# Kernel optimization log

Hardware: AMD Instinct MI355X
Metric: run time of the kernel (lower is better)

The kernel has to match this reference:

```python
import jax, jax.numpy as jnp
import numpy as np

B = 64          # batch of graphs
N_GOALS = 16
N_SHELVES = 112
N = N_GOALS + N_SHELVES   # 128 nodes per graph
L = 5           # num_layers
D = 32          # node_embedding_dim
DE = 32         # edge_embedding_dim
DT = 32         # timestep_embedding_dim
D_MSG_IN = 2 * D + DT + 1  # 97


def setup_inputs() -> dict:
    key = jax.random.key(0)
    ks = iter(jax.random.split(key, 40))
    def nrm(shape, s=0.05):
        return jax.random.normal(next(ks), shape, jnp.float32) * s
    inp = {}
    inp["pos"] = jax.random.uniform(next(ks), (B, N_SHELVES, 2), jnp.float32, -1.0, 1.0)
    inp["timesteps"] = jax.random.randint(next(ks), (B,), 0, 1000)
    inp["goal_pos"] = jax.random.uniform(next(ks), (N_GOALS, 2), jnp.float32, -1.0, 1.0)
    inp["W_hin"] = nrm((2, D));            inp["b_hin"] = nrm((D,))
    inp["W_msg1"] = nrm((L, D_MSG_IN, DE)); inp["b_msg1"] = nrm((L, DE))
    inp["W_msg2"] = nrm((L, DE, DE));       inp["b_msg2"] = nrm((L, DE))
    inp["W_att"] = nrm((L, DE, 1));         inp["b_att"] = nrm((L, 1))
    inp["W_pos1"] = nrm((L, DE, DE));       inp["b_pos1"] = nrm((L, DE))
    inp["W_pos2"] = nrm((L, DE, 1));        inp["b_pos2"] = nrm((L, 1))
    inp["W_node1"] = nrm((L - 1, DE + D, D)); inp["b_node1"] = nrm((L - 1, D))
    inp["W_node2"] = nrm((L - 1, D, D));      inp["b_node2"] = nrm((L - 1, D))
    inp["W_t"] = nrm((L - 1, DT, DT));        inp["b_t"] = nrm((L - 1, DT))
    return inp


def _forward(pos, timesteps, goal_pos, W_hin, b_hin, W_msg1, b_msg1, W_msg2, b_msg2,
             W_att, b_att, W_pos1, b_pos1, W_pos2, b_pos2,
             W_node1, b_node1, W_node2, b_node2, W_t, b_t):
    silu = jax.nn.silu
    b = pos.shape[0]
    n_g = goal_pos.shape[0]
    n_sh = pos.shape[1]
    n = n_g + n_sh
    num_layers = W_msg1.shape[0]

    # fully-connected edge template per graph (PyG: edge_index[0]=src=row, edge_index[1]=dst=col)
    src_l = jnp.repeat(jnp.arange(n), n)
    dst_l = jnp.tile(jnp.arange(n), n)
    offs = (jnp.arange(b) * n)[:, None]
    src = (offs + src_l[None, :]).reshape(-1)   # [b*n*n]
    dst = (offs + dst_l[None, :]).reshape(-1)
    e_batch = jnp.repeat(jnp.arange(b), n * n)  # batch[edge_index[0]]

    # node one-hot features: goals [1,0], shelves [0,1]
    h0 = jnp.concatenate([
        jnp.tile(jnp.array([1.0, 0.0], jnp.float32), (n_g, 1)),
        jnp.tile(jnp.array([0.0, 1.0], jnp.float32), (n_sh, 1)),
    ], axis=0)                                   # [n, 2]
    x = jnp.tile(h0, (b, 1))                     # [b*n, 2]

    # node positions: goal positions (shared template) then shelf positions
    p = jnp.concatenate([jnp.broadcast_to(goal_pos, (b, n_g, 2)), pos], axis=1).reshape(-1, 2)

    # sinusoidal timestep embedding
    dt = b_t.shape[-1]
    half = dt // 2
    freqs = jnp.exp(-jnp.log(10000.0) * jnp.arange(half, dtype=jnp.float32) / half)
    ang = timesteps.astype(jnp.float32)[:, None] * freqs[None, :]
    temb = jnp.concatenate([jnp.cos(ang), jnp.sin(ang)], axis=-1)  # [b, dt]

    h = x @ W_hin + b_hin  # [b*n, D]

    for i in range(num_layers):
        te = temb[e_batch]                       # [E, dt]
        pd = p[dst] - p[src]                     # pos_i - pos_j
        radial = jnp.sum(pd * pd, axis=-1, keepdims=True)
        pd = pd / (jax.lax.stop_gradient(jnp.sqrt(radial)) + 1e-6)
        m = jnp.concatenate([h[dst], h[src], radial, te], axis=-1)  # [E, 97]
        m = silu(m @ W_msg1[i] + b_msg1[i])
        m = silu(m @ W_msg2[i] + b_msg2[i])
        m = m * jax.nn.sigmoid(m @ W_att[i] + b_att[i])             # attention gate
        pw = silu(m @ W_pos1[i] + b_pos1[i]) @ W_pos2[i] + b_pos2[i]  # [E, 1]
        aggr_h = jax.ops.segment_sum(m, dst, num_segments=b * n)    # scatter-add
        # scatter-mean: every node receives exactly n incoming edges (fully connected incl. self-loop)
        aggr_p = jax.ops.segment_sum(pd * pw, dst, num_segments=b * n) / n
        if i < num_layers - 1:
            u = silu(jnp.concatenate([h, aggr_h], axis=-1) @ W_node1[i] + b_node1[i])
            u = u @ W_node2[i] + b_node2[i]
            h = jnp.where(u > 0, u, 0.01 * u) + h   # LeakyReLU + residual
            temb = silu(temb @ W_t[i] + b_t[i])
        p = aggr_p + p

    return p.reshape(b, n, 2)[:, n_g:, :].reshape(pos.shape)


def reference(pos, timesteps, goal_pos, W_hin, b_hin, W_msg1, b_msg1, W_msg2, b_msg2,
              W_att, b_att, W_pos1, b_pos1, W_pos2, b_pos2,
              W_node1, b_node1, W_node2, b_node2, W_t, b_t):
    return _forward(pos, timesteps, goal_pos, W_hin, b_hin, W_msg1, b_msg1, W_msg2, b_msg2,
                    W_att, b_att, W_pos1, b_pos1, W_pos2, b_pos2,
                    W_node1, b_node1, W_node2, b_node2, W_t, b_t)
```

## Files before the change

### kernel.cpp

```cpp
#include <hip/hip_runtime.h>
#include <hip/hip_bf16.h>

constexpr int B = 64;
constexpr int NG = 16;
constexpr int NSH = 112;
constexpr int N = 128;
constexpr int NN = B * N;
constexpr int L = 5;

constexpr int OFF_H     = 0;
constexpr int OFF_P     = OFF_H + NN * 32;
constexpr int OFF_TEMB0 = OFF_P + NN * 2;
constexpr int OFF_TEMB1 = OFF_TEMB0 + B * 32;
constexpr int OFF_HA    = OFF_TEMB1 + B * 32;
constexpr int OFF_HB    = OFF_HA + NN * 32;
constexpr int OFF_AGH   = OFF_HB + NN * 32;
constexpr int OFF_AGP   = OFF_AGH + NN * 32;

typedef __attribute__((ext_vector_type(8))) short bf16x8;
typedef __attribute__((ext_vector_type(4))) float f32x4;

__device__ __forceinline__ float fsigmoid(float x) {
    return __builtin_amdgcn_rcpf(1.0f + __expf(-x));
}
__device__ __forceinline__ float fsilu(float x) { return x * fsigmoid(x); }
__device__ __forceinline__ short f2bfs(float f) {
    union { __hip_bfloat16 b; short s; } u; u.b = __float2bfloat16(f); return u.s;
}
__device__ __forceinline__ float bf2f(unsigned short u) {
    union { unsigned int i; float f; } v; v.i = ((unsigned int)u) << 16; return v.f;
}
__device__ __forceinline__ unsigned int pk_trunc(float lo, float hi) {
    union { float f; unsigned int u; } a, b;
    a.f = hi; b.f = lo;
    return __builtin_amdgcn_perm(a.u, b.u, 0x07060302u);
}

__global__ __launch_bounds__(256) void setup_kernel(
    const float* __restrict__ pos, const int* __restrict__ timesteps,
    const float* __restrict__ goal_pos,
    const float* __restrict__ W_hin, const float* __restrict__ b_hin,
    float* __restrict__ ws)
{
    int idx = blockIdx.x * 256 + threadIdx.x;

    if (idx < NN * 32) {
        int c = idx & 31; int node = idx >> 5; int local = node & 127;
        int row = (local < NG) ? 0 : 1;
        ws[OFF_H + idx] = W_hin[row * 32 + c] + b_hin[c];
        return;
    }
    idx -= NN * 32;
    if (idx < NN * 2) {
        int d = idx & 1; int node = idx >> 1; int g = node >> 7; int local = node & 127;
        float v = (local < NG) ? goal_pos[local * 2 + d]
                               : pos[(g * NSH + (local - NG)) * 2 + d];
        ws[OFF_P + idx] = v;
        return;
    }
    idx -= NN * 2;
    if (idx < B * 32) {
        int j = idx & 31; int g = idx >> 5;
        float t = (float)timesteps[g];
        int jj = (j < 16) ? j : (j - 16);
        float freq = expf(-logf(10000.0f) * (float)jj / 16.0f);
        float ang = t * freq;
        ws[OFF_TEMB0 + idx] = (j < 16) ? cosf(ang) : sinf(ang);
    }
}

__global__ __launch_bounds__(256) void pre_kernel(
    float* __restrict__ R,
    const float* __restrict__ W_msg1, const float* __restrict__ b_msg1,
    const float* __restrict__ tembIn, int layer)
{
    int tid = blockIdx.x * 256 + threadIdx.x;
    int c = tid & 31; int node = tid >> 5; int g = node >> 7;
    const float* __restrict__ W1 = W_msg1 + layer * 97 * 32;
    float accA = b_msg1[layer * 32 + c];
    float accB = 0.f;
#pragma unroll
    for (int k = 0; k < 32; ++k) {
        float hk = R[OFF_H + node * 32 + k];
        accA += hk * W1[k * 32 + c];
        accB += hk * W1[(32 + k) * 32 + c];
    }
#pragma unroll
    for (int k = 0; k < 32; ++k)
        accA += tembIn[g * 32 + k] * W1[(65 + k) * 32 + c];
    R[OFF_HA + tid] = accA;
    ((unsigned short*)(R + OFF_HB))[tid] = (unsigned short)f2bfs(accB);
}

__global__ __attribute__((amdgpu_flat_work_group_size(256, 256)))
__attribute__((amdgpu_waves_per_eu(2, 4))) void edge_kernel(
    float* __restrict__ R,
    const float* __restrict__ W_msg1,
    const float* __restrict__ W_msg2, const float* __restrict__ b_msg2,
    const float* __restrict__ W_att, const float* __restrict__ b_att,
    const float* __restrict__ W_pos1, const float* __restrict__ b_pos1,
    const float* __restrict__ W_pos2, const float* __restrict__ b_pos2,
    float* __restrict__ aggh, float* __restrict__ aggp,
    float* __restrict__ out, int layer)
{
    __shared__ unsigned short sHBh[128 * 40];
    __shared__ float sPx[128], sPy[128];
    __shared__ unsigned int mbuf[4 * 16 * 20];
    __shared__ float2 spn[4][64];

    const int t = threadIdx.x;
    const int bx = blockIdx.x;
    const int g = bx >> 5;
    const int gbase = g * 128;

    const unsigned short* HBH = (const unsigned short*)(R + OFF_HB);
#pragma unroll
    for (int ch = 0; ch < 2; ++ch) {
        int chunk = t + ch * 256;
        int row = chunk >> 2, g4 = chunk & 3;
        uint4 v = *(const uint4*)(HBH + (gbase + row) * 32 + (g4 << 3));
        *(uint4*)(sHBh + row * 40 + (g4 << 3)) = v;
    }
    if (t < 128) {
        sPx[t] = R[OFF_P + (gbase + t) * 2];
        sPy[t] = R[OFF_P + (gbase + t) * 2 + 1];
    }
    __syncthreads();

    const int lane = t & 63, w = t >> 6;
    const int c = lane & 15;
    const int rg = lane >> 4;
    const int kk = rg << 3;
    const int dloc = ((bx & 31) << 2) | w;
    const int dstNode = gbase + dloc;

    const float* __restrict__ Wm2L = W_msg2 + layer * 1024;
    const float* __restrict__ Wp1L = W_pos1 + layer * 1024;
    bf16x8 WB1c0, WB1c1, WBpc0, WBpc1, WBac;
#pragma unroll
    for (int j = 0; j < 8; ++j) {
        WB1c0[j] = f2bfs(Wm2L[(kk + j) * 32 + c]);
        WB1c1[j] = f2bfs(Wm2L[(kk + j) * 32 + c + 16]);
        int pk = ((kk + j) & 1) * 16 + ((kk + j) >> 1);
        WBpc0[j] = f2bfs(Wp1L[pk * 32 + c]);
        WBpc1[j] = f2bfs(Wp1L[pk * 32 + c + 16]);
        WBac[j]  = f2bfs(W_att[layer * 32 + pk]);
    }

    float vha[8], vwr[8];
    {
        const float* haR = R + OFF_HA + dstNode * 32 + kk;
        const float* wrR = W_msg1 + layer * 97 * 32 + 64 * 32 + kk;
#pragma unroll
        for (int j = 0; j < 8; ++j) { vha[j] = haR[j]; vwr[j] = wrR[j]; }
    }
    const float batt   = b_att[layer];
    const float vbm20  = b_msg2[layer * 32 + c], vbm21 = b_msg2[layer * 32 + c + 16];
    const float vbp10  = b_pos1[layer * 32 + c], vbp11 = b_pos1[layer * 32 + c + 16];
    const float vwp20  = W_pos2[layer * 32 + c], vwp21 = W_pos2[layer * 32 + c + 16];
    const float bp2    = b_pos2[layer];
    const float pxd = R[OFF_P + dstNode * 2], pyd = R[OFF_P + dstNode * 2 + 1];

    unsigned int* mb = mbuf + w * 16 * 20;

    float aghc0 = 0.f, aghc1 = 0.f, apx = 0.f, apy = 0.f, spnx = 0.f, spny = 0.f;

#pragma unroll 1
    for (int half = 0; half < 2; ++half) {
        const int src = (half << 6) + lane;
        const float dx = pxd - sPx[src];
        const float dy = pyd - sPy[src];
        const float radial = dx * dx + dy * dy;
        const float inv = __builtin_amdgcn_rcpf(__builtin_amdgcn_sqrtf(radial) + 1e-6f);
        const float pnx = dx * inv, pny = dy * inv;
        spnx += pnx; spny += pny;
        spn[w][lane] = (float2){pnx, pny};

#pragma unroll
        for (int tt = 0; tt < 4; ++tt) {
            const float rad_t = __shfl(radial, c + (tt << 4));
            uint4 hraw = *(const uint4*)(sHBh + ((half << 6) + c + (tt << 4)) * 40 + kk);
            const unsigned short* hs = (const unsigned short*)&hraw;
            float x[8];
#pragma unroll
            for (int j = 0; j < 8; ++j)
                x[j] = fsilu(vha[j] + bf2f(hs[j]) + rad_t * vwr[j]);
            union { unsigned int u[4]; bf16x8 v; } af;
#pragma unroll
            for (int d = 0; d < 4; ++d) af.u[d] = pk_trunc(x[2 * d], x[2 * d + 1]);
            f32x4 a0 = (f32x4){vbm20, vbm20, vbm20, vbm20};
            f32x4 a1 = (f32x4){vbm21, vbm21, vbm21, vbm21};
            a0 = __builtin_amdgcn_mfma_f32_16x16x32_bf16(af.v, WB1c0, a0, 0, 0, 0);
            a1 = __builtin_amdgcn_mfma_f32_16x16x32_bf16(af.v, WB1c1, a1, 0, 0, 0);

            float s0[4], s1[4];
#pragma unroll
            for (int j = 0; j < 4; ++j) {
                s0[j] = fsilu(a0[j]);
                s1[j] = fsilu(a1[j]);
                mb[((rg << 2) + j) * 20 + c] = pk_trunc(s0[j], s1[j]);
            }

            union { uint4 u; bf16x8 v; } qa;
            qa.u = *(const uint4*)(mb + c * 20 + (rg << 2));
            f32x4 za = (f32x4){batt, batt, batt, batt};
            f32x4 z0 = (f32x4){0.f, 0.f, 0.f, 0.f};
            f32x4 z1 = (f32x4){0.f, 0.f, 0.f, 0.f};
            za = __builtin_amdgcn_mfma_f32_16x16x32_bf16(qa.v, WBac,  za, 0, 0, 0);
            z0 = __builtin_amdgcn_mfma_f32_16x16x32_bf16(qa.v, WBpc0, z0, 0, 0, 0);
            z1 = __builtin_amdgcn_mfma_f32_16x16x32_bf16(qa.v, WBpc1, z1, 0, 0, 0);
#pragma unroll
            for (int j = 0; j < 4; ++j) {
                const float att = fsigmoid(za[j]);
                aghc0 += att * s0[j];
                aghc1 += att * s1[j];
                const float q0 = fsilu(att * z0[j] + vbp10);
                const float q1 = fsilu(att * z1[j] + vbp11);
                const float pwp = q0 * vwp20 + q1 * vwp21;
                const float2 pn = spn[w][(tt << 4) + (rg << 2) + j];
                apx += pwp * pn.x;
                apy += pwp * pn.y;
            }
        }
    }

    aghc0 += __shfl_xor(aghc0, 16); aghc0 += __shfl_xor(aghc0, 32);
    aghc1 += __shfl_xor(aghc1, 16); aghc1 += __shfl_xor(aghc1, 32);
#pragma unroll
    for (int off = 1; off < 64; off <<= 1) {
        apx  += __shfl_xor(apx, off);
        apy  += __shfl_xor(apy, off);
        spnx += __shfl_xor(spnx, off);
        spny += __shfl_xor(spny, off);
    }
    if (layer < L - 1) {
        if (lane < 16)       aggh[dstNode * 32 + lane] = aghc0;
        else if (lane < 32)  aggh[dstNode * 32 + lane] = aghc1;
        if (lane == 0) {
            aggp[dstNode * 2]     = (apx + bp2 * spnx) * (1.0f / 128.0f);
            aggp[dstNode * 2 + 1] = (apy + bp2 * spny) * (1.0f / 128.0f);
        }
    } else if (lane == 0 && dloc >= NG) {
        out[(g * NSH + (dloc - NG)) * 2]     = pxd + (apx + bp2 * spnx) * (1.0f / 128.0f);
        out[(g * NSH + (dloc - NG)) * 2 + 1] = pyd + (apy + bp2 * spny) * (1.0f / 128.0f);
    }
}

__global__ __attribute__((amdgpu_flat_work_group_size(64, 64)))
__attribute__((amdgpu_waves_per_eu(2, 4))) void node_kernel(
    float* __restrict__ ws,
    const float* __restrict__ W_node1, const float* __restrict__ b_node1,
    const float* __restrict__ W_node2, const float* __restrict__ b_node2,
    const float* __restrict__ W_t, const float* __restrict__ b_t,
    const float* __restrict__ W_msg1, const float* __restrict__ b_msg1,
    int layer)
{
    __shared__ float sH[16][36];
    __shared__ float sAG[16][36];
    __shared__ unsigned int mb[16 * 20];

    const int lane = threadIdx.x;
    const int bx = blockIdx.x;
    const int nbase = bx << 4;
    const int g = bx >> 3;
    const int c = lane & 15, rg = lane >> 4, kk = rg << 3;

    {
        const int row = lane >> 2, seg = lane & 3;
        const float* hsrc = ws + OFF_H + (nbase + row) * 32 + (seg << 3);
        const float* asrc = ws + OFF_AGH + (nbase + row) * 32 + (seg << 3);
#pragma unroll
        for (int j = 0; j < 8; ++j) {
            sH[row][(seg << 3) + j]  = hsrc[j];
            sAG[row][(seg << 3) + j] = asrc[j];
        }
    }

    const float* __restrict__ Wn1 = W_node1 + layer * 2048;
    const float* __restrict__ Wn2 = W_node2 + layer * 1024;
    const float* __restrict__ W1  = W_msg1 + (layer + 1) * 97 * 32;
    bf16x8 B1[2][2], B2[2], Ba[2], Bb[2];
#pragma unroll
    for (int j = 0; j < 8; ++j) {
        const int pk = ((kk + j) & 1) * 16 + ((kk + j) >> 1);
#pragma unroll
        for (int nh = 0; nh < 2; ++nh) {
            B1[0][nh][j] = f2bfs(Wn1[(kk + j) * 32 + nh * 16 + c]);
            B1[1][nh][j] = f2bfs(Wn1[(32 + kk + j) * 32 + nh * 16 + c]);
            B2[nh][j]    = f2bfs(Wn2[pk * 32 + nh * 16 + c]);
            Ba[nh][j]    = f2bfs(W1[pk * 32 + nh * 16 + c]);
            Bb[nh][j]    = f2bfs(W1[(32 + pk) * 32 + nh * 16 + c]);
        }
    }

    const int c2 = lane & 31;
    const float* __restrict__ tin = ws + ((layer & 1) ? OFF_TEMB1 : OFF_TEMB0) + g * 32;
    const float* __restrict__ Wt = W_t + layer * 1024;
    float a2 = b_t[layer * 32 + c2];
#pragma unroll
    for (int k = 0; k < 32; ++k) a2 += tin[k] * Wt[k * 32 + c2];
    const float tnew = fsilu(a2);
    float tv = b_msg1[(layer + 1) * 32 + c2];
#pragma unroll
    for (int k = 0; k < 32; ++k) tv += __shfl(tnew, k) * W1[(65 + k) * 32 + c2];
    if ((bx & 7) == 0 && lane < 32)
        ws[((layer & 1) ? OFF_TEMB0 : OFF_TEMB1) + g * 32 + lane] = tnew;

    union { unsigned int u[4]; bf16x8 v; } A0, A1;
#pragma unroll
    for (int d = 0; d < 4; ++d) {
        A0.u[d] = pk_trunc(sH[c][kk + 2 * d],  sH[c][kk + 2 * d + 1]);
        A1.u[d] = pk_trunc(sAG[c][kk + 2 * d], sAG[c][kk + 2 * d + 1]);
    }
    f32x4 u1[2];
#pragma unroll
    for (int nh = 0; nh < 2; ++nh) {
        const float bb = b_node1[layer * 32 + nh * 16 + c];
        f32x4 acc = (f32x4){bb, bb, bb, bb};
        acc = __builtin_amdgcn_mfma_f32_16x16x32_bf16(A0.v, B1[0][nh], acc, 0, 0, 0);
        acc = __builtin_amdgcn_mfma_f32_16x16x32_bf16(A1.v, B1[1][nh], acc, 0, 0, 0);
        u1[nh] = acc;
    }

#pragma unroll
    for (int j = 0; j < 4; ++j)
        mb[((rg << 2) + j) * 20 + c] = pk_trunc(fsilu(u1[0][j]), fsilu(u1[1][j]));
    union { uint4 q; bf16x8 v; } qa;
    qa.q = *(const uint4*)(mb + c * 20 + (rg << 2));
    f32x4 u2[2];
#pragma unroll
    for (int nh = 0; nh < 2; ++nh) {
        const float bb = b_node2[layer * 32 + nh * 16 + c];
        f32x4 acc = (f32x4){bb, bb, bb, bb};
        u2[nh] = __builtin_amdgcn_mfma_f32_16x16x32_bf16(qa.v, B2[nh], acc, 0, 0, 0);
    }

    float hp0[4], hp1[4];
#pragma unroll
    for (int j = 0; j < 4; ++j) {
        const int row = (rg << 2) + j;
        const float h0 = sH[row][c], h1 = sH[row][c + 16];
        const float v0 = u2[0][j], v1 = u2[1][j];
        hp0[j] = (v0 > 0.f ? v0 : 0.01f * v0) + h0;
        hp1[j] = (v1 > 0.f ? v1 : 0.01f * v1) + h1;
        ws[OFF_H + (nbase + row) * 32 + c]      = hp0[j];
        ws[OFF_H + (nbase + row) * 32 + c + 16] = hp1[j];
        mb[row * 20 + c] = pk_trunc(hp0[j], hp1[j]);
    }

    qa.q = *(const uint4*)(mb + c * 20 + (rg << 2));
    f32x4 ha[2], hb[2];
    {
        f32x4 zz = (f32x4){0.f, 0.f, 0.f, 0.f};
#pragma unroll
        for (int nh = 0; nh < 2; ++nh) {
            ha[nh] = __builtin_amdgcn_mfma_f32_16x16x32_bf16(qa.v, Ba[nh], zz, 0, 0, 0);
            hb[nh] = __builtin_amdgcn_mfma_f32_16x16x32_bf16(qa.v, Bb[nh], zz, 0, 0, 0);
        }
    }
    const float tv0 = __shfl(tv, c), tv1 = __shfl(tv, c + 16);
    unsigned short* HBH = (unsigned short*)(ws + OFF_HB);
#pragma unroll
    for (int j = 0; j < 4; ++j) {
        const int node = nbase + (rg << 2) + j;
        ws[OFF_HA + node * 32 + c]      = ha[0][j] + tv0;
        ws[OFF_HA + node * 32 + c + 16] = ha[1][j] + tv1;
        HBH[node * 32 + c]      = (unsigned short)f2bfs(hb[0][j]);
        HBH[node * 32 + c + 16] = (unsigned short)f2bfs(hb[1][j]);
    }

    if (lane < 32) {
        const int node = nbase + (lane >> 1), d = lane & 1;
        ws[OFF_P + node * 2 + d] += ws[OFF_AGP + node * 2 + d];
    }
}

extern "C" void kernel_launch(void* const* d_in, const int* in_sizes, int n_in,
                              void* d_out, int out_size, void* d_ws, size_t ws_size,
                              hipStream_t stream)
{
    const float* pos      = (const float*)d_in[0];
    const int*   tsteps   = (const int*)d_in[1];
    const float* goal_pos = (const float*)d_in[2];
    const float* W_hin    = (const float*)d_in[3];
    const float* b_hin    = (const float*)d_in[4];
    const float* W_msg1   = (const float*)d_in[5];
    const float* b_msg1   = (const float*)d_in[6];
    const float* W_msg2   = (const float*)d_in[7];
    const float* b_msg2   = (const float*)d_in[8];
    const float* W_att    = (const float*)d_in[9];
    const float* b_att    = (const float*)d_in[10];
    const float* W_pos1   = (const float*)d_in[11];
    const float* b_pos1   = (const float*)d_in[12];
    const float* W_pos2   = (const float*)d_in[13];
    const float* b_pos2   = (const float*)d_in[14];
    const float* W_node1  = (const float*)d_in[15];
    const float* b_node1  = (const float*)d_in[16];
    const float* W_node2  = (const float*)d_in[17];
    const float* b_node2  = (const float*)d_in[18];
    const float* W_t      = (const float*)d_in[19];
    const float* b_t      = (const float*)d_in[20];

    float* ws = (float*)d_ws;

    constexpr int setup_threads = NN * 32 + NN * 2 + B * 32;
    setup_kernel<<<(setup_threads + 255) / 256, 256, 0, stream>>>(
        pos, tsteps, goal_pos, W_hin, b_hin, ws);
    pre_kernel<<<NN * 32 / 256, 256, 0, stream>>>(ws, W_msg1, b_msg1, ws + OFF_TEMB0, 0);

    for (int l = 0; l < L; ++l) {
        edge_kernel<<<2048, 256, 0, stream>>>(ws, W_msg1, W_msg2, b_msg2, W_att, b_att,
                                              W_pos1, b_pos1, W_pos2, b_pos2,
                                              ws + OFF_AGH, ws + OFF_AGP,
                                              (float*)d_out, l);
        if (l < L - 1)
            node_kernel<<<512, 64, 0, stream>>>(ws, W_node1, b_node1, W_node2,
                                                b_node2, W_t, b_t, W_msg1, b_msg1, l);
    }
}
```

Baseline: 293.4 us.

## Fuse node update into edge kernel and merge setup with pre-projection

Fuses the per-layer node update into the tail of the edge kernel. Each block now handles 16 destination nodes, looping over four per wave, and keeps the aggregates in shared memory instead of writing them to global buffers. HA, HB and position buffers are double-buffered by layer parity so one block's writes do not race with other blocks' reads. The setup and first-layer pre-projection kernels are merged, which removes kernel launches and global round trips. In exchange the grid shrinks from 2048 to 512 blocks, with a serial loop over destinations and a 64-thread node-update tail, so parallelism drops.

Result: faster. 287.2 us, median of 2 (-2.1%).

```diff
diff --git a/kernel.cpp b/kernel.cpp
--- a/kernel.cpp
+++ b/kernel.cpp
@@ -9,13 +9,14 @@
 constexpr int L = 5;
 
 constexpr int OFF_H     = 0;
-constexpr int OFF_P     = OFF_H + NN * 32;
-constexpr int OFF_TEMB0 = OFF_P + NN * 2;
+constexpr int OFF_P0    = OFF_H + NN * 32;
+constexpr int OFF_P1    = OFF_P0 + NN * 2;
+constexpr int OFF_TEMB0 = OFF_P1 + NN * 2;
 constexpr int OFF_TEMB1 = OFF_TEMB0 + B * 32;
-constexpr int OFF_HA    = OFF_TEMB1 + B * 32;
-constexpr int OFF_HB    = OFF_HA + NN * 32;
-constexpr int OFF_AGH   = OFF_HB + NN * 32;
-constexpr int OFF_AGP   = OFF_AGH + NN * 32;
+constexpr int OFF_HA0   = OFF_TEMB1 + B * 32;
+constexpr int OFF_HA1   = OFF_HA0 + NN * 32;
+constexpr int OFF_HB0   = OFF_HA1 + NN * 32;
+constexpr int OFF_HB1   = OFF_HB0 + NN * 16;
 
 typedef __attribute__((ext_vector_type(8))) short bf16x8;
 typedef __attribute__((ext_vector_type(4))) float f32x4;
@@ -36,342 +37,337 @@
     return __builtin_amdgcn_perm(a.u, b.u, 0x07060302u);
 }
 
-__global__ __launch_bounds__(256) void setup_kernel(
-    const float* __restrict__ pos, const int* __restrict__ timesteps,
+__global__ __launch_bounds__(256) void setup_pre_kernel(
+    float* __restrict__ ws,
+    const float* __restrict__ pos, const int* __restrict__ tsteps,
     const float* __restrict__ goal_pos,
     const float* __restrict__ W_hin, const float* __restrict__ b_hin,
-    float* __restrict__ ws)
+    const float* __restrict__ W_msg1, const float* __restrict__ b_msg1)
 {
-    int idx = blockIdx.x * 256 + threadIdx.x;
-
-    if (idx < NN * 32) {
-        int c = idx & 31; int node = idx >> 5; int local = node & 127;
-        int row = (local < NG) ? 0 : 1;
-        ws[OFF_H + idx] = W_hin[row * 32 + c] + b_hin[c];
-        return;
-    }
-    idx -= NN * 32;
-    if (idx < NN * 2) {
-        int d = idx & 1; int node = idx >> 1; int g = node >> 7; int local = node & 127;
-        float v = (local < NG) ? goal_pos[local * 2 + d]
-                               : pos[(g * NSH + (local - NG)) * 2 + d];
-        ws[OFF_P + idx] = v;
-        return;
-    }
-    idx -= NN * 2;
-    if (idx < B * 32) {
-        int j = idx & 31; int g = idx >> 5;
-        float t = (float)timesteps[g];
-        int jj = (j < 16) ? j : (j - 16);
-        float freq = expf(-logf(10000.0f) * (float)jj / 16.0f);
-        float ang = t * freq;
-        ws[OFF_TEMB0 + idx] = (j < 16) ? cosf(ang) : sinf(ang);
-    }
-}
-
-__global__ __launch_bounds__(256) void pre_kernel(
-    float* __restrict__ R,
-    const float* __restrict__ W_msg1, const float* __restrict__ b_msg1,
-    const float* __restrict__ tembIn, int layer)
-{
-    int tid = blockIdx.x * 256 + threadIdx.x;
-    int c = tid & 31; int node = tid >> 5; int g = node >> 7;
-    const float* __restrict__ W1 = W_msg1 + layer * 97 * 32;
-    float accA = b_msg1[layer * 32 + c];
-    float accB = 0.f;
+    __shared__ float sT[32];
+    const int t = threadIdx.x, bx = blockIdx.x;
+    const int tid = bx * 256 + t;
+    const int c = tid & 31, node = tid >> 5, g = node >> 7, local = node & 127;
+    const int row = (local < NG) ? 0 : 1;
+
+    if (t < 32) {
+        const float tf = (float)tsteps[g];
+        const int jj = (t < 16) ? t : (t - 16);
+        const float ang = tf * expf(-logf(10000.0f) * (float)jj / 16.0f);
+        sT[t] = (t < 16) ? cosf(ang) : sinf(ang);
+    }
+    __syncthreads();
+    if ((bx & 15) == 0 && t < 32) ws[OFF_TEMB0 + g * 32 + t] = sT[t];
+
+    ws[OFF_H + tid] = W_hin[row * 32 + c] + b_hin[c];
+
+    if (tid < NN * 2) {
+        const int d = tid & 1, nd = tid >> 1, g0 = nd >> 7, loc = nd & 127;
+        ws[OFF_P0 + tid] = (loc < NG) ? goal_pos[loc * 2 + d]
+                                      : pos[(g0 * NSH + (loc - NG)) * 2 + d];
+    }
+
+    const float* __restrict__ W1 = W_msg1;
+    float accA = b_msg1[c], accB = 0.f;
 #pragma unroll
     for (int k = 0; k < 32; ++k) {
-        float hk = R[OFF_H + node * 32 + k];
+        const float hk = W_hin[row * 32 + k] + b_hin[k];
         accA += hk * W1[k * 32 + c];
         accB += hk * W1[(32 + k) * 32 + c];
     }
 #pragma unroll
     for (int k = 0; k < 32; ++k)
-        accA += tembIn[g * 32 + k] * W1[(65 + k) * 32 + c];
-    R[OFF_HA + tid] = accA;
-    ((unsigned short*)(R + OFF_HB))[tid] = (unsigned short)f2bfs(accB);
+        accA += sT[k] * W1[(65 + k) * 32 + c];
+    ws[OFF_HA0 + tid] = accA;
+    ((unsigned short*)(ws + OFF_HB0))[tid] = (unsigned short)f2bfs(accB);
 }
 
 __global__ __attribute__((amdgpu_flat_work_group_size(256, 256)))
 __attribute__((amdgpu_waves_per_eu(2, 4))) void edge_kernel(
-    float* __restrict__ R,
-    const float* __restrict__ W_msg1,
+    float* __restrict__ ws,
+    const float* __restrict__ W_msg1, const float* __restrict__ b_msg1,
     const float* __restrict__ W_msg2, const float* __restrict__ b_msg2,
     const float* __restrict__ W_att, const float* __restrict__ b_att,
     const float* __restrict__ W_pos1, const float* __restrict__ b_pos1,
     const float* __restrict__ W_pos2, const float* __restrict__ b_pos2,
-    float* __restrict__ aggh, float* __restrict__ aggp,
-    float* __restrict__ out, int layer)
+    const float* __restrict__ W_node1, const float* __restrict__ b_node1,
+    const float* __restrict__ W_node2, const float* __restrict__ b_node2,
+    const float* __restrict__ W_t, const float* __restrict__ b_t,
+    float* __restrict__ out, int l)
 {
     __shared__ unsigned short sHBh[128 * 40];
     __shared__ float sPx[128], sPy[128];
-    __shared__ unsigned int mbuf[4 * 16 * 20];
-    __shared__ float2 spn[4][64];
+    __shared__ __align__(16) unsigned char uraw[7168];
+    __shared__ float sAgg[16][36];
+    __shared__ float2 sAgp[16];
+
+    unsigned int* mbuf = (unsigned int*)uraw;
+    float2* spn = (float2*)(uraw + 5120);
+    float (*sH)[36] = (float(*)[36])uraw;
+    unsigned int* nmb = (unsigned int*)(uraw + 2304);
 
     const int t = threadIdx.x;
     const int bx = blockIdx.x;
-    const int g = bx >> 5;
-    const int gbase = g * 128;
-
-    const unsigned short* HBH = (const unsigned short*)(R + OFF_HB);
+    const int g = bx >> 3, qp = bx & 7;
+    const int gbase = g << 7;
+    const int par = l & 1, op = (l + 1) & 1;
+
+    const float* __restrict__ HAin = ws + (par ? OFF_HA1 : OFF_HA0);
+    const unsigned short* __restrict__ HBin = (const unsigned short*)(ws + (par ? OFF_HB1 : OFF_HB0));
+    const float* __restrict__ Pin = ws + (par ? OFF_P1 : OFF_P0);
+
 #pragma unroll
     for (int ch = 0; ch < 2; ++ch) {
-        int chunk = t + ch * 256;
-        int row = chunk >> 2, g4 = chunk & 3;
-        uint4 v = *(const uint4*)(HBH + (gbase + row) * 32 + (g4 << 3));
-        *(uint4*)(sHBh + row * 40 + (g4 << 3)) = v;
+        const int chunk = t + (ch << 8);
+        const int row = chunk >> 2, g4 = chunk & 3;
+        *(uint4*)(sHBh + row * 40 + (g4 << 3)) =
+            *(const uint4*)(HBin + (gbase + row) * 32 + (g4 << 3));
     }
     if (t < 128) {
-        sPx[t] = R[OFF_P + (gbase + t) * 2];
-        sPy[t] = R[OFF_P + (gbase + t) * 2 + 1];
+        sPx[t] = Pin[(gbase + t) * 2];
+        sPy[t] = Pin[(gbase + t) * 2 + 1];
     }
     __syncthreads();
 
     const int lane = t & 63, w = t >> 6;
-    const int c = lane & 15;
-    const int rg = lane >> 4;
-    const int kk = rg << 3;
-    const int dloc = ((bx & 31) << 2) | w;
-    const int dstNode = gbase + dloc;
-
-    const float* __restrict__ Wm2L = W_msg2 + layer * 1024;
-    const float* __restrict__ Wp1L = W_pos1 + layer * 1024;
+    const int c = lane & 15, rg = lane >> 4, kk = rg << 3;
+
+    const float* __restrict__ Wm2L = W_msg2 + l * 1024;
+    const float* __restrict__ Wp1L = W_pos1 + l * 1024;
     bf16x8 WB1c0, WB1c1, WBpc0, WBpc1, WBac;
 #pragma unroll
     for (int j = 0; j < 8; ++j) {
         WB1c0[j] = f2bfs(Wm2L[(kk + j) * 32 + c]);
         WB1c1[j] = f2bfs(Wm2L[(kk + j) * 32 + c + 16]);
-        int pk = ((kk + j) & 1) * 16 + ((kk + j) >> 1);
+        const int pk = ((kk + j) & 1) * 16 + ((kk + j) >> 1);
         WBpc0[j] = f2bfs(Wp1L[pk * 32 + c]);
         WBpc1[j] = f2bfs(Wp1L[pk * 32 + c + 16]);
-        WBac[j]  = f2bfs(W_att[layer * 32 + pk]);
-    }
-
-    float vha[8], vwr[8];
+        WBac[j]  = f2bfs(W_att[l * 32 + pk]);
+    }
+    float vwr[8];
     {
-        const float* haR = R + OFF_HA + dstNode * 32 + kk;
-        const float* wrR = W_msg1 + layer * 97 * 32 + 64 * 32 + kk;
-#pragma unroll
-        for (int j = 0; j < 8; ++j) { vha[j] = haR[j]; vwr[j] = wrR[j]; }
-    }
-    const float batt   = b_att[layer];
-    const float vbm20  = b_msg2[layer * 32 + c], vbm21 = b_msg2[layer * 32 + c + 16];
-    const float vbp10  = b_pos1[layer * 32 + c], vbp11 = b_pos1[layer * 32 + c + 16];
-    const float vwp20  = W_pos2[layer * 32 + c], vwp21 = W_pos2[layer * 32 + c + 16];
-    const float bp2    = b_pos2[layer];
-    const float pxd = R[OFF_P + dstNode * 2], pyd = R[OFF_P + dstNode * 2 + 1];
+        const float* wrR = W_msg1 + l * 97 * 32 + 64 * 32 + kk;
+#pragma unroll
+        for (int j = 0; j < 8; ++j) vwr[j] = wrR[j];
+    }
+    const float batt  = b_att[l];
+    const float vbm20 = b_msg2[l * 32 + c], vbm21 = b_msg2[l * 32 + c + 16];
+    const float vbp10 = b_pos1[l * 32 + c], vbp11 = b_pos1[l * 32 + c + 16];
+    const float vwp20 = W_pos2[l * 32 + c], vwp21 = W_pos2[l * 32 + c + 16];
+    const float bp2   = b_pos2[l];
 
     unsigned int* mb = mbuf + w * 16 * 20;
 
-    float aghc0 = 0.f, aghc1 = 0.f, apx = 0.f, apy = 0.f, spnx = 0.f, spny = 0.f;
-
 #pragma unroll 1
-    for (int half = 0; half < 2; ++half) {
-        const int src = (half << 6) + lane;
-        const float dx = pxd - sPx[src];
-        const float dy = pyd - sPy[src];
-        const float radial = dx * dx + dy * dy;
-        const float inv = __builtin_amdgcn_rcpf(__builtin_amdgcn_sqrtf(radial) + 1e-6f);
-        const float pnx = dx * inv, pny = dy * inv;
-        spnx += pnx; spny += pny;
-        spn[w][lane] = (float2){pnx, pny};
-
-#pragma unroll
-        for (int tt = 0; tt < 4; ++tt) {
-            const float rad_t = __shfl(radial, c + (tt << 4));
-            uint4 hraw = *(const uint4*)(sHBh + ((half << 6) + c + (tt << 4)) * 40 + kk);
-            const unsigned short* hs = (const unsigned short*)&hraw;
-            float x[8];
-#pragma unroll
-            for (int j = 0; j < 8; ++j)
-                x[j] = fsilu(vha[j] + bf2f(hs[j]) + rad_t * vwr[j]);
-            union { unsigned int u[4]; bf16x8 v; } af;
-#pragma unroll
-            for (int d = 0; d < 4; ++d) af.u[d] = pk_trunc(x[2 * d], x[2 * d + 1]);
-            f32x4 a0 = (f32x4){vbm20, vbm20, vbm20, vbm20};
-            f32x4 a1 = (f32x4){vbm21, vbm21, vbm21, vbm21};
-            a0 = __builtin_amdgcn_mfma_f32_16x16x32_bf16(af.v, WB1c0, a0, 0, 0, 0);
-            a1 = __builtin_amdgcn_mfma_f32_16x16x32_bf16(af.v, WB1c1, a1, 0, 0, 0);
-
-            float s0[4], s1[4];
-#pragma unroll
-            for (int j = 0; j < 4; ++j) {
-                s0[j] = fsilu(a0[j]);
-                s1[j] = fsilu(a1[j]);
-                mb[((rg << 2) + j) * 20 + c] = pk_trunc(s0[j], s1[j]);
+    for (int si = 0; si < 4; ++si) {
+        const int dl = (si << 2) + w;
+        const int dloc = (qp << 4) + dl;
+        const int dstNode = gbase + dloc;
+        float vha[8];
+        {
+            const float* haR = HAin + dstNode * 32 + kk;
+#pragma unroll
+            for (int j = 0; j < 8; ++j) vha[j] = haR[j];
+        }
+        const float pxd = sPx[dloc], pyd = sPy[dloc];
+
+        float aghc0 = 0.f, aghc1 = 0.f, apx = 0.f, apy = 0.f;
+        float spnx = 0.f, spny = 0.f;
+
+#pragma unroll 1
+        for (int half = 0; half < 2; ++half) {
+            const int src = (half << 6) + lane;
+            const float dx = pxd - sPx[src];
+            const float dy = pyd - sPy[src];
+            const float radial = dx * dx + dy * dy;
+            const float inv = __builtin_amdgcn_rcpf(__builtin_amdgcn_sqrtf(radial) + 1e-6f);
+            const float pnx = dx * inv, pny = dy * inv;
+            spnx += pnx; spny += pny;
+            spn[w * 64 + lane] = (float2){pnx, pny};
+
+#pragma unroll
+            for (int tt = 0; tt < 4; ++tt) {
+                const float rad_t = __shfl(radial, c + (tt << 4));
+                uint4 hraw = *(const uint4*)(sHBh + ((half << 6) + c + (tt << 4)) * 40 + kk);
+                const unsigned short* hs = (const unsigned short*)&hraw;
+                float x[8];
+#pragma unroll
+                for (int j = 0; j < 8; ++j)
+                    x[j] = fsilu(vha[j] + bf2f(hs[j]) + rad_t * vwr[j]);
+                union { unsigned int u[4]; bf16x8 v; } af;
+#pragma unroll
+                for (int d = 0; d < 4; ++d) af.u[d] = pk_trunc(x[2 * d], x[2 * d + 1]);
+                f32x4 a0 = (f32x4){vbm20, vbm20, vbm20, vbm20};
+                f32x4 a1 = (f32x4){vbm21, vbm21, vbm21, vbm21};
+                a0 = __builtin_amdgcn_mfma_f32_16x16x32_bf16(af.v, WB1c0, a0, 0, 0, 0);
+                a1 = __builtin_amdgcn_mfma_f32_16x16x32_bf16(af.v, WB1c1, a1, 0, 0, 0);
+
+                float s0[4], s1[4];
+#pragma unroll
+                for (int j = 0; j < 4; ++j) {
+                    s0[j] = fsilu(a0[j]);
+                    s1[j] = fsilu(a1[j]);
+                    mb[((rg << 2) + j) * 20 + c] = pk_trunc(s0[j], s1[j]);
+                }
+
+                union { uint4 u; bf16x8 v; } qa;
+                qa.u = *(const uint4*)(mb + c * 20 + (rg << 2));
+                f32x4 za = (f32x4){batt, batt, batt, batt};
+                f32x4 z0 = (f32x4){0.f, 0.f, 0.f, 0.f};
+                f32x4 z1 = (f32x4){0.f, 0.f, 0.f, 0.f};
+                za = __builtin_amdgcn_mfma_f32_16x16x32_bf16(qa.v, WBac,  za, 0, 0, 0);
+                z0 = __builtin_amdgcn_mfma_f32_16x16x32_bf16(qa.v, WBpc0, z0, 0, 0, 0);
+                z1 = __builtin_amdgcn_mfma_f32_16x16x32_bf16(qa.v, WBpc1, z1, 0, 0, 0);
+#pragma unroll
+                for (int j = 0; j < 4; ++j) {
+                    const float att = fsigmoid(za[j]);
+                    aghc0 += att * s0[j];
+                    aghc1 += att * s1[j];
+                    const float q0 = fsilu(att * z0[j] + vbp10);
+                    const float q1 = fsilu(att * z1[j] + vbp11);
+                    const float pwp = q0 * vwp20 + q1 * vwp21;
+                    const float2 pn = spn[w * 64 + (tt << 4) + (rg << 2) + j];
+                    apx += pwp * pn.x;
+                    apy += pwp * pn.y;
+                }
             }
-
-            union { uint4 u; bf16x8 v; } qa;
-            qa.u = *(const uint4*)(mb + c * 20 + (rg << 2));
-            f32x4 za = (f32x4){batt, batt, batt, batt};
-            f32x4 z0 = (f32x4){0.f, 0.f, 0.f, 0.f};
-            f32x4 z1 = (f32x4){0.f, 0.f, 0.f, 0.f};
-            za = __builtin_amdgcn_mfma_f32_16x16x32_bf16(qa.v, WBac,  za, 0, 0, 0);
-            z0 = __builtin_amdgcn_mfma_f32_16x16x32_bf16(qa.v, WBpc0, z0, 0, 0, 0);
-            z1 = __builtin_amdgcn_mfma_f32_16x16x32_bf16(qa.v, WBpc1, z1, 0, 0, 0);
-#pragma unroll
-            for (int j = 0; j < 4; ++j) {
-                const float att = fsigmoid(za[j]);
-                aghc0 += att * s0[j];
-                aghc1 += att * s1[j];
-                const float q0 = fsilu(att * z0[j] + vbp10);
-                const float q1 = fsilu(att * z1[j] + vbp11);
-                const float pwp = q0 * vwp20 + q1 * vwp21;
-                const float2 pn = spn[w][(tt << 4) + (rg << 2) + j];
-                apx += pwp * pn.x;
-                apy += pwp * pn.y;
+        }
+
+        aghc0 += __shfl_xor(aghc0, 16); aghc0 += __shfl_xor(aghc0, 32);
+        aghc1 += __shfl_xor(aghc1, 16); aghc1 += __shfl_xor(aghc1, 32);
+#pragma unroll
+        for (int off = 1; off < 64; off <<= 1) {
+            apx  += __shfl_xor(apx, off);
+            apy  += __shfl_xor(apy, off);
+            spnx += __shfl_xor(spnx, off);
+            spny += __shfl_xor(spny, off);
+        }
+        if (l < L - 1) {
+            if (lane < 32) sAgg[dl][lane] = (lane < 16) ? aghc0 : aghc1;
+            if (lane == 0)
+                sAgp[dl] = (float2){(apx + bp2 * spnx) * (1.0f / 128.0f),
+                                    (apy + bp2 * spny) * (1.0f / 128.0f)};
+        } else if (lane == 0 && dloc >= NG) {
+            out[(g * NSH + (dloc - NG)) * 2]     = pxd + (apx + bp2 * spnx) * (1.0f / 128.0f);
+            out[(g * NSH + (dloc - NG)) * 2 + 1] = pyd + (apy + bp2 * spny) * (1.0f / 128.0f);
+        }
+    }
+    if (l == L - 1) return;
+
+    __syncthreads();
+
+    if (t < 64) {
+        const int nbase = bx << 4;
+        float* __restrict__ HAout = ws + (op ? OFF_HA1 : OFF_HA0);
+        unsigned short* __restrict__ HBout = (unsigned short*)(ws + (op ? OFF_HB1 : OFF_HB0));
+        float* __restrict__ Pout = ws + (op ? OFF_P1 : OFF_P0);
+
+        {
+            const int row = lane >> 2, seg = lane & 3;
+            const float* hsrc = ws + OFF_H + (nbase + row) * 32 + (seg << 3);
+#pragma unroll
+            for (int j = 0; j < 8; ++j) sH[row][(seg << 3) + j] = hsrc[j];
+        }
+
+        const float* __restrict__ Wn1 = W_node1 + l * 2048;
+        const float* __restrict__ Wn2 = W_node2 + l * 1024;
+        const float* __restrict__ W1  = W_msg1 + (l + 1) * 97 * 32;
+        bf16x8 B1[2][2], B2[2], Ba[2], Bb[2];
+#pragma unroll
+        for (int j = 0; j < 8; ++j) {
+            const int pk = ((kk + j) & 1) * 16 + ((kk + j) >> 1);
+#pragma unroll
+            for (int nh = 0; nh < 2; ++nh) {
+                B1[0][nh][j] = f2bfs(Wn1[(kk + j) * 32 + nh * 16 + c]);
+                B1[1][nh][j] = f2bfs(Wn1[(32 + kk + j) * 32 + nh * 16 + c]);
+                B2[nh][j]    = f2bfs(Wn2[pk * 32 + nh * 16 + c]);
+                Ba[nh][j]    = f2bfs(W1[pk * 32 + nh * 16 + c]);
+                Bb[nh][j]    = f2bfs(W1[(32 + pk) * 32 + nh * 16 + c]);
             }
         }
-    }
-
-    aghc0 += __shfl_xor(aghc0, 16); aghc0 += __shfl_xor(aghc0, 32);
-    aghc1 += __shfl_xor(aghc1, 16); aghc1 += __shfl_xor(aghc1, 32);
-#pragma unroll
-    for (int off = 1; off < 64; off <<= 1) {
-        apx  += __shfl_xor(apx, off);
-        apy  += __shfl_xor(apy, off);
-        spnx += __shfl_xor(spnx, off);
-        spny += __shfl_xor(spny, off);
-    }
-    if (layer < L - 1) {
-        if (lane < 16)       aggh[dstNode * 32 + lane] = aghc0;
-        else if (lane < 32)  aggh[dstNode * 32 + lane] = aghc1;
-        if (lane == 0) {
-            aggp[dstNode * 2]     = (apx + bp2 * spnx) * (1.0f / 128.0f);
-            aggp[dstNode * 2 + 1] = (apy + bp2 * spny) * (1.0f / 128.0f);
-        }
-    } else if (lane == 0 && dloc >= NG) {
-        out[(g * NSH + (dloc - NG)) * 2]     = pxd + (apx + bp2 * spnx) * (1.0f / 128.0f);
-        out[(g * NSH + (dloc - NG)) * 2 + 1] = pyd + (apy + bp2 * spny) * (1.0f / 128.0f);
-    }
-}
-
-__global__ __attribute__((amdgpu_flat_work_group_size(64, 64)))
-__attribute__((amdgpu_waves_per_eu(2, 4))) void node_kernel(
-    float* __restrict__ ws,
-    const float* __restrict__ W_node1, const float* __restrict__ b_node1,
-    const float* __restrict__ W_node2, const float* __restrict__ b_node2,
-    const float* __restrict__ W_t, const float* __restrict__ b_t,
-    const float* __restrict__ W_msg1, const float* __restrict__ b_msg1,
-    int layer)
-{
-    __shared__ float sH[16][36];
-    __shared__ float sAG[16][36];
-    __shared__ unsigned int mb[16 * 20];
-
-    const int lane = threadIdx.x;
-    const int bx = blockIdx.x;
-    const int nbase = bx << 4;
-    const int g = bx >> 3;
-    const int c = lane & 15, rg = lane >> 4, kk = rg << 3;
-
-    {
-        const int row = lane >> 2, seg = lane & 3;
-        const float* hsrc = ws + OFF_H + (nbase + row) * 32 + (seg << 3);
-        const float* asrc = ws + OFF_AGH + (nbase + row) * 32 + (seg << 3);
-#pragma unroll
-        for (int j = 0; j < 8; ++j) {
-            sH[row][(seg << 3) + j]  = hsrc[j];
-            sAG[row][(seg << 3) + j] = asrc[j];
-        }
-    }
-
-    const float* __restrict__ Wn1 = W_node1 + layer * 2048;
-    const float* __restrict__ Wn2 = W_node2 + layer * 1024;
-    const float* __restrict__ W1  = W_msg1 + (layer + 1) * 97 * 32;
-    bf16x8 B1[2][2], B2[2], Ba[2], Bb[2];
-#pragma unroll
-    for (int j = 0; j < 8; ++j) {
-        const int pk = ((kk + j) & 1) * 16 + ((kk + j) >> 1);
+
+        const int c2 = lane & 31;
+        const float* __restrict__ tin = ws + (par ? OFF_TEMB1 : OFF_TEMB0) + g * 32;
+        const float* __restrict__ Wt = W_t + l * 1024;
+        float a2 = b_t[l * 32 + c2];
+#pragma unroll
+        for (int k = 0; k < 32; ++k) a2 += tin[k] * Wt[k * 32 + c2];
+        const float tnew = fsilu(a2);
+        float tv = b_msg1[(l + 1) * 32 + c2];
+#pragma unroll
+        for (int k = 0; k < 32; ++k) tv += __shfl(tnew, k) * W1[(65 + k) * 32 + c2];
+        if ((bx & 7) == 0 && lane < 32)
+            ws[(par ? OFF_TEMB0 : OFF_TEMB1) + g * 32 + lane] = tnew;
+
+        union { unsigned int u[4]; bf16x8 v; } A0, A1;
+#pragma unroll
+        for (int d = 0; d < 4; ++d) {
+            A0.u[d] = pk_trunc(sH[c][kk + 2 * d],   sH[c][kk + 2 * d + 1]);
+            A1.u[d] = pk_trunc(sAgg[c][kk + 2 * d], sAgg[c][kk + 2 * d + 1]);
+        }
+        f32x4 u1[2];
 #pragma unroll
         for (int nh = 0; nh < 2; ++nh) {
-            B1[0][nh][j] = f2bfs(Wn1[(kk + j) * 32 + nh * 16 + c]);
-            B1[1][nh][j] = f2bfs(Wn1[(32 + kk + j) * 32 + nh * 16 + c]);
-            B2[nh][j]    = f2bfs(Wn2[pk * 32 + nh * 16 + c]);
-            Ba[nh][j]    = f2bfs(W1[pk * 32 + nh * 16 + c]);
-            Bb[nh][j]    = f2bfs(W1[(32 + pk) * 32 + nh * 16 + c]);
-        }
-    }
-
-    const int c2 = lane & 31;
-    const float* __restrict__ tin = ws + ((layer & 1) ? OFF_TEMB1 : OFF_TEMB0) + g * 32;
-    const float* __restrict__ Wt = W_t + layer * 1024;
-    float a2 = b_t[layer * 32 + c2];
-#pragma unroll
-    for (int k = 0; k < 32; ++k) a2 += tin[k] * Wt[k * 32 + c2];
-    const float tnew = fsilu(a2);
-    float tv = b_msg1[(layer + 1) * 32 + c2];
-#pragma unroll
-    for (int k = 0; k < 32; ++k) tv += __shfl(tnew, k) * W1[(65 + k) * 32 + c2];
-    if ((bx & 7) == 0 && lane < 32)
-        ws[((layer & 1) ? OFF_TEMB0 : OFF_TEMB1) + g * 32 + lane] = tnew;
-
-    union { unsigned int u[4]; bf16x8 v; } A0, A1;
-#pragma unroll
-    for (int d = 0; d < 4; ++d) {
-        A0.u[d] = pk_trunc(sH[c][kk + 2 * d],  sH[c][kk + 2 * d + 1]);
-        A1.u[d] = pk_trunc(sAG[c][kk + 2 * d], sAG[c][kk + 2 * d + 1]);
-    }
-    f32x4 u1[2];
-#pragma unroll
-    for (int nh = 0; nh < 2; ++nh) {
-        const float bb = b_node1[layer * 32 + nh * 16 + c];
-        f32x4 acc = (f32x4){bb, bb, bb, bb};
-        acc = __builtin_amdgcn_mfma_f32_16x16x32_bf16(A0.v, B1[0][nh], acc, 0, 0, 0);
-        acc = __builtin_amdgcn_mfma_f32_16x16x32_bf16(A1.v, B1[1][nh], acc, 0, 0, 0);
-        u1[nh] = acc;
-    }
-
-#pragma unroll
-    for (int j = 0; j < 4; ++j)
-        mb[((rg << 2) + j) * 20 + c] = pk_trunc(fsilu(u1[0][j]), fsilu(u1[1][j]));
-    union { uint4 q; bf16x8 v; } qa;
-    qa.q = *(const uint4*)(mb + c * 20 + (rg << 2));
-    f32x4 u2[2];
-#pragma unroll
-    for (int nh = 0; nh < 2; ++nh) {
-        const float bb = b_node2[layer * 32 + nh * 16 + c];
-        f32x4 acc = (f32x4){bb, bb, bb, bb};
-        u2[nh] = __builtin_amdgcn_mfma_f32_16x16x32_bf16(qa.v, B2[nh], acc, 0, 0, 0);
-    }
-
-    float hp0[4], hp1[4];
-#pragma unroll
-    for (int j = 0; j < 4; ++j) {
-        const int row = (rg << 2) + j;
-        const float h0 = sH[row][c], h1 = sH[row][c + 16];
-        const float v0 = u2[0][j], v1 = u2[1][j];
-        hp0[j] = (v0 > 0.f ? v0 : 0.01f * v0) + h0;
-        hp1[j] = (v1 > 0.f ? v1 : 0.01f * v1) + h1;
-        ws[OFF_H + (nbase + row) * 32 + c]      = hp0[j];
-        ws[OFF_H + (nbase + row) * 32 + c + 16] = hp1[j];
-        mb[row * 20 + c] = pk_trunc(hp0[j], hp1[j]);
-    }
-
-    qa.q = *(const uint4*)(mb + c * 20 + (rg << 2));
-    f32x4 ha[2], hb[2];
-    {
-        f32x4 zz = (f32x4){0.f, 0.f, 0.f, 0.f};
+            const float bb = b_node1[l * 32 + nh * 16 + c];
+            f32x4 acc = (f32x4){bb, bb, bb, bb};
+            acc = __builtin_amdgcn_mfma_f32_16x16x32_bf16(A0.v, B1[0][nh], acc, 0, 0, 0);
+            acc = __builtin_amdgcn_mfma_f32_16x16x32_bf16(A1.v, B1[1][nh], acc, 0, 0, 0);
+            u1[nh] = acc;
+        }
+
+#pragma unroll
+        for (int j = 0; j < 4; ++j)
+            nmb[((rg << 2) + j) * 20 + c] = pk_trunc(fsilu(u1[0][j]), fsilu(u1[1][j]));
+        union { uint4 q; bf16x8 v; } qa;
+        qa.q = *(const uint4*)(nmb + c * 20 + (rg << 2));
+        f32x4 u2[2];
 #pragma unroll
         for (int nh = 0; nh < 2; ++nh) {
-            ha[nh] = __builtin_amdgcn_mfma_f32_16x16x32_bf16(qa.v, Ba[nh], zz, 0, 0, 0);
-            hb[nh] = __builtin_amdgcn_mfma_f32_16x16x32_bf16(qa.v, Bb[nh], zz, 0, 0, 0);
-        }
-    }
-    const float tv0 = __shfl(tv, c), tv1 = __shfl(tv, c + 16);
-    unsigned short* HBH = (unsigned short*)(ws + OFF_HB);
-#pragma unroll
-    for (int j = 0; j < 4; ++j) {
-        const int node = nbase + (rg << 2) + j;
-        ws[OFF_HA + node * 32 + c]      = ha[0][j] + tv0;
-        ws[OFF_HA + node * 32 + c + 16] = ha[1][j] + tv1;
-        HBH[node * 32 + c]      = (unsigned short)f2bfs(hb[0][j]);
-        HBH[node * 32 + c + 16] = (unsigned short)f2bfs(hb[1][j]);
-    }
-
-    if (lane < 32) {
-        const int node = nbase + (lane >> 1), d = lane & 1;
-        ws[OFF_P + node * 2 + d] += ws[OFF_AGP + node * 2 + d];
+            const float bb = b_node2[l * 32 + nh * 16 + c];
+            f32x4 acc = (f32x4){bb, bb, bb, bb};
+            u2[nh] = __builtin_amdgcn_mfma_f32_16x16x32_bf16(qa.v, B2[nh], acc, 0, 0, 0);
+        }
+
+        float hp0[4], hp1[4];
+#pragma unroll
+        for (int j = 0; j < 4; ++j) {
+            const int row = (rg << 2) + j;
+            const float h0 = sH[row][c], h1 = sH[row][c + 16];
+            const float v0 = u2[0][j], v1 = u2[1][j];
+            hp0[j] = (v0 > 0.f ? v0 : 0.01f * v0) + h0;
+            hp1[j] = (v1 > 0.f ? v1 : 0.01f * v1) + h1;
+            ws[OFF_H + (nbase + row) * 32 + c]      = hp0[j];
+            ws[OFF_H + (nbase + row) * 32 + c + 16] = hp1[j];
+            nmb[row * 20 + c] = pk_trunc(hp0[j], hp1[j]);
+        }
+
+        qa.q = *(const uint4*)(nmb + c * 20 + (rg << 2));
+        f32x4 ha[2], hb[2];
+        {
+            f32x4 zz = (f32x4){0.f, 0.f, 0.f, 0.f};
+#pragma unroll
+            for (int nh = 0; nh < 2; ++nh) {
+                ha[nh] = __builtin_amdgcn_mfma_f32_16x16x32_bf16(qa.v, Ba[nh], zz, 0, 0, 0);
+                hb[nh] = __builtin_amdgcn_mfma_f32_16x16x32_bf16(qa.v, Bb[nh], zz, 0, 0, 0);
+            }
+        }
+        const float tv0 = __shfl(tv, c), tv1 = __shfl(tv, c + 16);
+#pragma unroll
+        for (int j = 0; j < 4; ++j) {
+            const int node = nbase + (rg << 2) + j;
+            HAout[node * 32 + c]      = ha[0][j] + tv0;
+            HAout[node * 32 + c + 16] = ha[1][j] + tv1;
+            HBout[node * 32 + c]      = (unsigned short)f2bfs(hb[0][j]);
+            HBout[node * 32 + c + 16] = (unsigned short)f2bfs(hb[1][j]);
+        }
+
+        if (lane < 32) {
+            const int dl2 = lane >> 1, d = lane & 1;
+            const int node = nbase + dl2;
+            const float ag = d ? sAgp[dl2].y : sAgp[dl2].x;
+            Pout[node * 2 + d] = (par ? ws[OFF_P1 + node * 2 + d]
+                                      : ws[OFF_P0 + node * 2 + d]) + ag;
+        }
     }
 }
 
@@ -403,18 +399,13 @@
 
     float* ws = (float*)d_ws;
 
-    constexpr int setup_threads = NN * 32 + NN * 2 + B * 32;
-    setup_kernel<<<(setup_threads + 255) / 256, 256, 0, stream>>>(
-        pos, tsteps, goal_pos, W_hin, b_hin, ws);
-    pre_kernel<<<NN * 32 / 256, 256, 0, stream>>>(ws, W_msg1, b_msg1, ws + OFF_TEMB0, 0);
-
-    for (int l = 0; l < L; ++l) {
-        edge_kernel<<<2048, 256, 0, stream>>>(ws, W_msg1, W_msg2, b_msg2, W_att, b_att,
-                                              W_pos1, b_pos1, W_pos2, b_pos2,
-                                              ws + OFF_AGH, ws + OFF_AGP,
-                                              (float*)d_out, l);
-        if (l < L - 1)
-            node_kernel<<<512, 64, 0, stream>>>(ws, W_node1, b_node1, W_node2,
-                                                b_node2, W_t, b_t, W_msg1, b_msg1, l);
-    }
-}
+    setup_pre_kernel<<<1024, 256, 0, stream>>>(ws, pos, tsteps, goal_pos,
+                                               W_hin, b_hin, W_msg1, b_msg1);
+
+    for (int l = 0; l < L; ++l)
+        edge_kernel<<<512, 256, 0, stream>>>(ws, W_msg1, b_msg1, W_msg2, b_msg2,
+                                             W_att, b_att, W_pos1, b_pos1,
+                                             W_pos2, b_pos2, W_node1, b_node1,
+                                             W_node2, b_node2, W_t, b_t,
+                                             (float*)d_out, l);
+}
```
